# Kernel optimization log

Measured on AMD Instinct MI355X. Metric: run time of the kernel, lower is better.

Reference implementation:

```python
import jax, jax.numpy as jnp
import numpy as np

N = 50000   # nodes
E = 800000  # edges (avg degree 16)
D = 64      # isize == hidden_dim
L = 3       # num_gc_layers
BN_EPS = 1e-5


def setup_inputs() -> dict:
    key = jax.random.key(0)
    ks = jax.random.split(key, 8)
    x = jax.random.normal(ks[0], (N, D), dtype=jnp.float32)
    edge_index = jax.random.randint(ks[1], (2, E), 0, N, dtype=jnp.int64)
    # Stacked per-layer MLP params (layer 0 has isize==hidden_dim so shapes match)
    scale = 0.05
    W1 = jax.random.normal(ks[2], (L, D, D), dtype=jnp.float32) * scale
    b1 = jax.random.normal(ks[3], (L, D), dtype=jnp.float32) * scale
    W2 = jax.random.normal(ks[4], (L, D, D), dtype=jnp.float32) * scale
    b2 = jax.random.normal(ks[5], (L, D), dtype=jnp.float32) * scale
    gamma = jnp.ones((L, D), dtype=jnp.float32)
    beta = jnp.zeros((L, D), dtype=jnp.float32)
    return {"x": x, "edge_index": edge_index, "W1": W1, "b1": b1,
            "W2": W2, "b2": b2, "gamma": gamma, "beta": beta}


def reference(x, edge_index, W1, b1, W2, b2, gamma, beta):
    # GINConv (eps=0): h_i' = MLP(x_i + sum_{j->i} x_j), then BatchNorm1d
    # (training-mode batch statistics), ReLU on all but the last layer.
    # Dropout is identity (deterministic / eval).
    src = edge_index[0]
    dst = edge_index[1]
    h = x
    for i in range(L):
        agg = jax.ops.segment_sum(h[src], dst, num_segments=N)  # [N, D] scatter-add
        z = h + agg                                             # (1+eps)*x + agg, eps=0
        z = jnp.maximum(z @ W1[i] + b1[i], 0.0)                 # MLP hidden + ReLU
        z = z @ W2[i] + b2[i]                                   # MLP out
        mean = jnp.mean(z, axis=0)
        var = jnp.var(z, axis=0)                                # biased var, as torch BN
        z = (z - mean) * jax.lax.rsqrt(var + BN_EPS) * gamma[i] + beta[i]
        if i < L - 1:
            z = jnp.maximum(z, 0.0)
        h = z
    return h
```

## Files before the change

### kernel.cpp

```cpp
#include <hip/hip_runtime.h>

#define NN 50000
#define NPAD 50064
#define EE 800000
#define DD 64
#define BN_EPS 1e-5f

#define NPART 8
#define PART_NODES 6250
#define CAP 64
#define BCAP 131072
#define NSCAT 32
#define NB_BUCKET 782
#define NB_AGG  12500
#define NB_MLP  782
#define NB_SETUP 1563
#define NB_ELT8 1563
#define NB_APPLY 3125

typedef __attribute__((ext_vector_type(8))) short short8v;
typedef __attribute__((ext_vector_type(4))) float float4v;

__device__ __forceinline__ unsigned bfpack2(float a, float b) {
    union { float f; unsigned u; } ua, ub;
    ua.f = a; ub.f = b;
    unsigned ra = ua.u + 0x7fffu + ((ua.u >> 16) & 1u);
    unsigned rb = ub.u + 0x7fffu + ((ub.u >> 16) & 1u);
    return (ra >> 16) | (rb & 0xffff0000u);
}

__device__ __forceinline__ unsigned short bf16of(float v) {
    union { float f; unsigned u; } x; x.f = v;
    unsigned r = x.u + 0x7fffu + ((x.u >> 16) & 1u);
    return (unsigned short)(r >> 16);
}

__global__ __launch_bounds__(256) void k_setup(const float* __restrict__ x,
                                               unsigned* __restrict__ xb,
                                               const float* __restrict__ W1,
                                               const float* __restrict__ W2,
                                               unsigned short* __restrict__ Wb,
                                               int* __restrict__ bucketCnt,
                                               float* __restrict__ stats) {
    int t = blockIdx.x * 256 + threadIdx.x;
    if (t < NN * 8) {
        const float4* p = (const float4*)(x + (size_t)t * 8);
        float4 a = p[0], b = p[1];
        uint4 o;
        o.x = bfpack2(a.x, a.y); o.y = bfpack2(a.z, a.w);
        o.z = bfpack2(b.x, b.y); o.w = bfpack2(b.z, b.w);
        ((uint4*)xb)[t] = o;
    }
    if (t < 3 * 2 * 4096) {
        int l = t / 8192;
        int rem = t - l * 8192;
        int m = rem / 4096;
        int e = rem - m * 4096;
        int c = e >> 6, k = e & 63;
        const float* W = (m == 0 ? W1 : W2) + l * 4096;
        Wb[t] = bf16of(W[k * 64 + c]);
    }
    if (t < 128) bucketCnt[t] = 0;
    else if (t < 512) stats[t - 128] = 0.f;
}

__global__ __launch_bounds__(1024) void k_build(const int* __restrict__ src,
                                                const int* __restrict__ dst,
                                                unsigned long long* __restrict__ bucket,
                                                int* __restrict__ bucketCnt,
                                                int* __restrict__ cursor) {
    __shared__ int lcnt[8];
    __shared__ int lbase[8];
    int t = threadIdx.x;
    int g = blockIdx.x * 1024 + t;
    if (g < NN) cursor[g] = 0;
    if (t < 8) lcnt[t] = 0;
    __syncthreads();
    int d = 0, s = 0, p = 0, loc = 0;
    bool ok = (g < EE);
    if (ok) {
        d = __builtin_nontemporal_load(dst + g);
        s = __builtin_nontemporal_load(src + g);
        p = (unsigned)d / PART_NODES;
        loc = atomicAdd(&lcnt[p], 1);
    }
    __syncthreads();
    if (t < 8) lbase[t] = atomicAdd(&bucketCnt[t * 16], lcnt[t]);
    __syncthreads();
    if (ok) {
        unsigned long long v = ((unsigned long long)(unsigned)s << 32) | (unsigned)d;
        bucket[(size_t)p * BCAP + lbase[p] + loc] = v;
    }
}

__global__ __launch_bounds__(256) void k_scatter(const unsigned long long* __restrict__ bucket,
                                                 const int* __restrict__ bucketCnt,
                                                 int* __restrict__ cursor,
                                                 int* __restrict__ col) {
    int p = blockIdx.x & 7;
    int cnt = bucketCnt[p * 16];
    const unsigned long long* b = bucket + (size_t)p * BCAP;
    for (int i = (blockIdx.x >> 3) * 256 + threadIdx.x; i < cnt; i += NSCAT * 256) {
        unsigned long long v = __builtin_nontemporal_load(b + i);
        int d = (int)(v & 0xffffffffu);
        int s = (int)(v >> 32);
        int pos = atomicAdd(&cursor[d], 1);
        col[d * CAP + pos] = s;
    }
}

__global__ __launch_bounds__(256) void k_agg4(const unsigned* __restrict__ hb,
                                              const int* __restrict__ deg,
                                              const int* __restrict__ col,
                                              unsigned* __restrict__ outZb) {
    int node = blockIdx.x * 4 + (threadIdx.x >> 6);
    int lane = threadIdx.x & 63;
    int li = lane & 7;
    int slot = lane >> 3;
    int dn = deg[node];
    int base = node * CAP;
    const uint4* hb4 = (const uint4*)hb;
    float acc[8];
#pragma unroll
    for (int i = 0; i < 8; ++i) acc[i] = 0.f;

#define UNPK_ADD(U)                                                      \
    {                                                                    \
        uint4 _u = (U);                                                  \
        union { unsigned u; float f; } l0, h0, l1, h1, l2, h2, l3, h3;   \
        l0.u = _u.x << 16; h0.u = _u.x & 0xffff0000u;                    \
        l1.u = _u.y << 16; h1.u = _u.y & 0xffff0000u;                    \
        l2.u = _u.z << 16; h2.u = _u.z & 0xffff0000u;                    \
        l3.u = _u.w << 16; h3.u = _u.w & 0xffff0000u;                    \
        acc[0] += l0.f; acc[1] += h0.f; acc[2] += l1.f; acc[3] += h1.f;  \
        acc[4] += l2.f; acc[5] += h2.f; acc[6] += l3.f; acc[7] += h3.f;  \
    }

    if (slot == 0)
        UNPK_ADD(hb4[(size_t)node * 8 + li]);

    int k = slot;
    for (; k + 8 < dn; k += 16) {
        int s0 = __builtin_nontemporal_load(col + base + k);
        int s1 = __builtin_nontemporal_load(col + base + k + 8);
        uint4 u0 = hb4[(size_t)s0 * 8 + li];
        uint4 u1 = hb4[(size_t)s1 * 8 + li];
        UNPK_ADD(u0);
        UNPK_ADD(u1);
    }
    if (k < dn) {
        int s0 = __builtin_nontemporal_load(col + base + k);
        UNPK_ADD(hb4[(size_t)s0 * 8 + li]);
    }
#undef UNPK_ADD

#pragma unroll
    for (int i = 0; i < 8; ++i) acc[i] += __shfl_xor(acc[i], 8);
#pragma unroll
    for (int i = 0; i < 8; ++i) acc[i] += __shfl_xor(acc[i], 16);
#pragma unroll
    for (int i = 0; i < 8; ++i) acc[i] += __shfl_xor(acc[i], 32);

    if (slot == 0) {
        uint4 o;
        o.x = bfpack2(acc[0], acc[1]);
        o.y = bfpack2(acc[2], acc[3]);
        o.z = bfpack2(acc[4], acc[5]);
        o.w = bfpack2(acc[6], acc[7]);
        ((uint4*)outZb)[(size_t)node * 8 + li] = o;
    }
}

__global__ __launch_bounds__(256) void k_mlp_mfma(const unsigned short* __restrict__ Zb,
                                                  const unsigned short* __restrict__ WbL,
                                                  const float* __restrict__ b1,
                                                  const float* __restrict__ b2,
                                                  float* __restrict__ Zf,
                                                  float* __restrict__ statsL) {
    __shared__ unsigned short sm[4][16 * 72];
    __shared__ float sred[2][4][64];
    int w = threadIdx.x >> 6;
    int lane = threadIdx.x & 63;
    int q = lane >> 4;
    int cl = lane & 15;
    int r0 = blockIdx.x * 64 + w * 16;

    short8v B1[4][2], B2[4][2];
#pragma unroll
    for (int t = 0; t < 4; ++t) {
#pragma unroll
        for (int h = 0; h < 2; ++h) {
            B1[t][h] = *(const short8v*)(WbL + ((t * 16 + cl) * 64 + h * 32 + q * 8));
            B2[t][h] = *(const short8v*)(WbL + 4096 + ((t * 16 + cl) * 64 + h * 32 + q * 8));
        }
    }

    const unsigned short* zr = Zb + (size_t)(r0 + cl) * 64;
    short8v a0 = *(const short8v*)(zr + q * 8);
    short8v a1 = *(const short8v*)(zr + 32 + q * 8);

    float4v acc1[4];
#pragma unroll
    for (int t = 0; t < 4; ++t) {
        float b = b1[t * 16 + cl];
        acc1[t] = (float4v){b, b, b, b};
        acc1[t] = __builtin_amdgcn_mfma_f32_16x16x32_bf16(a0, B1[t][0], acc1[t], 0, 0, 0);
        acc1[t] = __builtin_amdgcn_mfma_f32_16x16x32_bf16(a1, B1[t][1], acc1[t], 0, 0, 0);
    }

    unsigned short* s = sm[w];
#pragma unroll
    for (int t = 0; t < 4; ++t) {
#pragma unroll
        for (int r = 0; r < 4; ++r) {
            float v = fmaxf(acc1[t][r], 0.f);
            s[(q * 4 + r) * 72 + t * 16 + cl] = bf16of(v);
        }
    }

    short8v a2_0 = *(const short8v*)(s + cl * 72 + q * 8);
    short8v a2_1 = *(const short8v*)(s + cl * 72 + 32 + q * 8);

    float4v acc2[4];
#pragma unroll
    for (int t = 0; t < 4; ++t) {
        float b = b2[t * 16 + cl];
        acc2[t] = (float4v){b, b, b, b};
        acc2[t] = __builtin_amdgcn_mfma_f32_16x16x32_bf16(a2_0, B2[t][0], acc2[t], 0, 0, 0);
        acc2[t] = __builtin_amdgcn_mfma_f32_16x16x32_bf16(a2_1, B2[t][1], acc2[t], 0, 0, 0);
    }

#pragma unroll
    for (int t = 0; t < 4; ++t) {
#pragma unroll
        for (int r = 0; r < 4; ++r) {
            int row = r0 + q * 4 + r;
            if (row < NN) Zf[(size_t)row * 64 + t * 16 + cl] = acc2[t][r];
        }
    }

#pragma unroll
    for (int t = 0; t < 4; ++t) {
        float sv = 0.f, qv = 0.f;
#pragma unroll
        for (int r = 0; r < 4; ++r) {
            int row = r0 + q * 4 + r;
            float v = (row < NN) ? acc2[t][r] : 0.f;
            sv += v;
            qv = fmaf(v, v, qv);
        }
        sv += __shfl_xor(sv, 16); sv += __shfl_xor(sv, 32);
        qv += __shfl_xor(qv, 16); qv += __shfl_xor(qv, 32);
        if (lane < 16) {
            sred[0][w][t * 16 + cl] = sv;
            sred[1][w][t * 16 + cl] = qv;
        }
    }
    __syncthreads();
    int tt = threadIdx.x;
    if (tt < 128) {
        int which = tt >> 6, c = tt & 63;
        float tot = sred[which][0][c] + sred[which][1][c] +
                    sred[which][2][c] + sred[which][3][c];
        atomicAdd(&statsL[which * 64 + c], tot);
    }
}

__global__ __launch_bounds__(256) void k_bnapply16(const float* __restrict__ Z,
                                                   const float* __restrict__ statsL,
                                                   const float* __restrict__ gammaL,
                                                   const float* __restrict__ betaL,
                                                   unsigned* __restrict__ hb) {
    __shared__ float sa[64];
    __shared__ float sc[64];
    int tt = threadIdx.x;
    if (tt < 64) {
        float mean = statsL[tt] * (1.f / NN);
        float var = statsL[64 + tt] * (1.f / NN) - mean * mean;
        float a = gammaL[tt] * rsqrtf(var + BN_EPS);
        sa[tt] = a;
        sc[tt] = fmaf(-mean, a, betaL[tt]);
    }
    __syncthreads();
    int t = blockIdx.x * 256 + tt;
    if (t >= NN * 8) return;
    int cb = (t & 7) * 8;
    const float4* p = (const float4*)(Z + (size_t)t * 8);
    float4 a = p[0], b = p[1];
    a.x = fmaxf(fmaf(a.x, sa[cb + 0], sc[cb + 0]), 0.f);
    a.y = fmaxf(fmaf(a.y, sa[cb + 1], sc[cb + 1]), 0.f);
    a.z = fmaxf(fmaf(a.z, sa[cb + 2], sc[cb + 2]), 0.f);
    a.w = fmaxf(fmaf(a.w, sa[cb + 3], sc[cb + 3]), 0.f);
    b.x = fmaxf(fmaf(b.x, sa[cb + 4], sc[cb + 4]), 0.f);
    b.y = fmaxf(fmaf(b.y, sa[cb + 5], sc[cb + 5]), 0.f);
    b.z = fmaxf(fmaf(b.z, sa[cb + 6], sc[cb + 6]), 0.f);
    b.w = fmaxf(fmaf(b.w, sa[cb + 7], sc[cb + 7]), 0.f);
    uint4 o;
    o.x = bfpack2(a.x, a.y); o.y = bfpack2(a.z, a.w);
    o.z = bfpack2(b.x, b.y); o.w = bfpack2(b.z, b.w);
    ((uint4*)hb)[t] = o;
}

__global__ __launch_bounds__(256) void k_apply_aff(const float* __restrict__ B,
                                                   const float* __restrict__ statsL,
                                                   const float* __restrict__ gammaL,
                                                   const float* __restrict__ betaL,
                                                   float* __restrict__ out) {
    __shared__ float sa[64];
    __shared__ float sc[64];
    int t = threadIdx.x;
    if (t < 64) {
        float mean = statsL[t] * (1.f / NN);
        float var = statsL[64 + t] * (1.f / NN) - mean * mean;
        float a = gammaL[t] * rsqrtf(var + BN_EPS);
        sa[t] = a;
        sc[t] = fmaf(-mean, a, betaL[t]);
    }
    __syncthreads();
    int i4 = blockIdx.x * 256 + t;
    if (i4 >= NN * 16) return;
    int cb = (i4 & 15) * 4;
    float4 v = ((const float4*)B)[i4];
    float4 o;
    o.x = fmaf(v.x, sa[cb + 0], sc[cb + 0]);
    o.y = fmaf(v.y, sa[cb + 1], sc[cb + 1]);
    o.z = fmaf(v.z, sa[cb + 2], sc[cb + 2]);
    o.w = fmaf(v.w, sa[cb + 3], sc[cb + 3]);
    ((float4*)out)[i4] = o;
}

extern "C" void kernel_launch(void* const* d_in, const int* in_sizes, int n_in,
                              void* d_out, int out_size, void* d_ws, size_t ws_size,
                              hipStream_t stream) {
    const float* x     = (const float*)d_in[0];
    const int*   ei    = (const int*)d_in[1];
    const float* W1    = (const float*)d_in[2];
    const float* b1    = (const float*)d_in[3];
    const float* W2    = (const float*)d_in[4];
    const float* b2    = (const float*)d_in[5];
    const float* gamma = (const float*)d_in[6];
    const float* beta  = (const float*)d_in[7];
    float* out = (float*)d_out;

    const int* src = ei;
    const int* dst = ei + EE;

    char* w = (char*)d_ws;
    unsigned*       Zb  = (unsigned*)w;       w += (size_t)NPAD * DD * 2;
    float*          Zf  = (float*)w;          w += (size_t)NN * DD * 4;
    unsigned*       Hb  = (unsigned*)w;       w += (size_t)NN * DD * 2;
    unsigned*       Xb  = (unsigned*)w;       w += (size_t)NN * DD * 2;
    int*            col = (int*)w;            w += (size_t)NN * CAP * 4;
    unsigned long long* bucket = (unsigned long long*)w;
    w += (size_t)NPART * BCAP * 8;
    int*            cursor    = (int*)w;      w += (size_t)NN * 4;
    int*            bucketCnt = (int*)w;      w += 128 * 4;
    float*          stats     = (float*)w;    w += 384 * 4;
    unsigned short* Wb        = (unsigned short*)w; w += 3 * 2 * 4096 * 2;

    k_setup<<<NB_SETUP, 256, 0, stream>>>(x, Xb, W1, W2, Wb, bucketCnt, stats);
    k_build<<<NB_BUCKET, 1024, 0, stream>>>(src, dst, bucket, bucketCnt, cursor);
    k_scatter<<<NPART * NSCAT, 256, 0, stream>>>(bucket, bucketCnt, cursor, col);

    k_agg4<<<NB_AGG, 256, 0, stream>>>(Xb, cursor, col, Zb);
    k_mlp_mfma<<<NB_MLP, 256, 0, stream>>>((unsigned short*)Zb, Wb, b1, b2, Zf, stats);
    k_bnapply16<<<NB_ELT8, 256, 0, stream>>>(Zf, stats, gamma, beta, Hb);

    k_agg4<<<NB_AGG, 256, 0, stream>>>(Hb, cursor, col, Zb);
    k_mlp_mfma<<<NB_MLP, 256, 0, stream>>>((unsigned short*)Zb, Wb + 8192, b1 + 64, b2 + 64, Zf, stats + 128);
    k_bnapply16<<<NB_ELT8, 256, 0, stream>>>(Zf, stats + 128, gamma + 64, beta + 64, Hb);

    k_agg4<<<NB_AGG, 256, 0, stream>>>(Hb, cursor, col, Zb);
    k_mlp_mfma<<<NB_MLP, 256, 0, stream>>>((unsigned short*)Zb, Wb + 16384, b1 + 128, b2 + 128, Zf, stats + 256);
    k_apply_aff<<<NB_APPLY, 256, 0, stream>>>(Zf, stats + 256, gamma + 128, beta + 128, out);
}
```

Before: 239.5 us.

## Fuse BatchNorm apply and ReLU into neighbor aggregation, store MLP output as bf16

Drops the separate BN-apply kernels for layers 0 and 1. The MLP kernel now writes its pre-BN output as bf16 through shared-memory staging. The next aggregation kernel then applies the affine BN and ReLU to every gathered neighbor row on the fly. This removes one full fp32 write plus read-and-write pass per layer and two launches. In exchange it adds per-edge FMA and max work, plus an extra bf16 rounding step before BN is applied.

```diff
diff --git a/kernel.cpp b/kernel.cpp
--- a/kernel.cpp
+++ b/kernel.cpp
@@ -15,7 +15,6 @@
 #define NB_AGG  12500
 #define NB_MLP  782
 #define NB_SETUP 1563
-#define NB_ELT8 1563
 #define NB_APPLY 3125
 
 typedef __attribute__((ext_vector_type(8))) short short8v;
@@ -109,10 +108,27 @@
     }
 }
 
+template<int FUSE>
 __global__ __launch_bounds__(256) void k_agg4(const unsigned* __restrict__ hb,
                                               const int* __restrict__ deg,
                                               const int* __restrict__ col,
+                                              const float* __restrict__ statsL,
+                                              const float* __restrict__ gammaL,
+                                              const float* __restrict__ betaL,
                                               unsigned* __restrict__ outZb) {
+    __shared__ float sa[64];
+    __shared__ float sc[64];
+    if (FUSE) {
+        int tt = threadIdx.x;
+        if (tt < 64) {
+            float mean = statsL[tt] * (1.f / NN);
+            float var = statsL[64 + tt] * (1.f / NN) - mean * mean;
+            float a = gammaL[tt] * rsqrtf(var + BN_EPS);
+            sa[tt] = a;
+            sc[tt] = fmaf(-mean, a, betaL[tt]);
+        }
+        __syncthreads();
+    }
     int node = blockIdx.x * 4 + (threadIdx.x >> 6);
     int lane = threadIdx.x & 63;
     int li = lane & 7;
@@ -120,6 +136,11 @@
     int dn = deg[node];
     int base = node * CAP;
     const uint4* hb4 = (const uint4*)hb;
+    float a8[8], c8[8];
+    if (FUSE) {
+#pragma unroll
+        for (int j = 0; j < 8; ++j) { a8[j] = sa[li * 8 + j]; c8[j] = sc[li * 8 + j]; }
+    }
     float acc[8];
 #pragma unroll
     for (int i = 0; i < 8; ++i) acc[i] = 0.f;
@@ -132,8 +153,10 @@
         l1.u = _u.y << 16; h1.u = _u.y & 0xffff0000u;                    \
         l2.u = _u.z << 16; h2.u = _u.z & 0xffff0000u;                    \
         l3.u = _u.w << 16; h3.u = _u.w & 0xffff0000u;                    \
-        acc[0] += l0.f; acc[1] += h0.f; acc[2] += l1.f; acc[3] += h1.f;  \
-        acc[4] += l2.f; acc[5] += h2.f; acc[6] += l3.f; acc[7] += h3.f;  \
+        float v[8] = {l0.f, h0.f, l1.f, h1.f, l2.f, h2.f, l3.f, h3.f};   \
+        _Pragma("unroll")                                                \
+        for (int j = 0; j < 8; ++j)                                      \
+            acc[j] += FUSE ? fmaxf(fmaf(v[j], a8[j], c8[j]), 0.f) : v[j];\
     }
 
     if (slot == 0)
@@ -171,10 +194,12 @@
     }
 }
 
+template<int OUTF32>
 __global__ __launch_bounds__(256) void k_mlp_mfma(const unsigned short* __restrict__ Zb,
                                                   const unsigned short* __restrict__ WbL,
                                                   const float* __restrict__ b1,
                                                   const float* __restrict__ b2,
+                                                  unsigned short* __restrict__ Mb,
                                                   float* __restrict__ Zf,
                                                   float* __restrict__ statsL) {
     __shared__ unsigned short sm[4][16 * 72];
@@ -230,12 +255,29 @@
         acc2[t] = __builtin_amdgcn_mfma_f32_16x16x32_bf16(a2_1, B2[t][1], acc2[t], 0, 0, 0);
     }
 
-#pragma unroll
-    for (int t = 0; t < 4; ++t) {
-#pragma unroll
-        for (int r = 0; r < 4; ++r) {
-            int row = r0 + q * 4 + r;
-            if (row < NN) Zf[(size_t)row * 64 + t * 16 + cl] = acc2[t][r];
+    if (OUTF32) {
+#pragma unroll
+        for (int t = 0; t < 4; ++t) {
+#pragma unroll
+            for (int r = 0; r < 4; ++r) {
+                int row = r0 + q * 4 + r;
+                if (row < NN) Zf[(size_t)row * 64 + t * 16 + cl] = acc2[t][r];
+            }
+        }
+    } else {
+#pragma unroll
+        for (int t = 0; t < 4; ++t) {
+#pragma unroll
+            for (int r = 0; r < 4; ++r) {
+                s[(q * 4 + r) * 72 + t * 16 + cl] = bf16of(acc2[t][r]);
+            }
+        }
+        short8v m0 = *(const short8v*)(s + cl * 72 + q * 8);
+        short8v m1 = *(const short8v*)(s + cl * 72 + 32 + q * 8);
+        int orow = r0 + cl;
+        if (orow < NN) {
+            *(short8v*)(Mb + (size_t)orow * 64 + q * 8) = m0;
+            *(short8v*)(Mb + (size_t)orow * 64 + 32 + q * 8) = m1;
         }
     }
 
@@ -264,41 +306,6 @@
                     sred[which][2][c] + sred[which][3][c];
         atomicAdd(&statsL[which * 64 + c], tot);
     }
-}
-
-__global__ __launch_bounds__(256) void k_bnapply16(const float* __restrict__ Z,
-                                                   const float* __restrict__ statsL,
-                                                   const float* __restrict__ gammaL,
-                                                   const float* __restrict__ betaL,
-                                                   unsigned* __restrict__ hb) {
-    __shared__ float sa[64];
-    __shared__ float sc[64];
-    int tt = threadIdx.x;
-    if (tt < 64) {
-        float mean = statsL[tt] * (1.f / NN);
-        float var = statsL[64 + tt] * (1.f / NN) - mean * mean;
-        float a = gammaL[tt] * rsqrtf(var + BN_EPS);
-        sa[tt] = a;
-        sc[tt] = fmaf(-mean, a, betaL[tt]);
-    }
-    __syncthreads();
-    int t = blockIdx.x * 256 + tt;
-    if (t >= NN * 8) return;
-    int cb = (t & 7) * 8;
-    const float4* p = (const float4*)(Z + (size_t)t * 8);
-    float4 a = p[0], b = p[1];
-    a.x = fmaxf(fmaf(a.x, sa[cb + 0], sc[cb + 0]), 0.f);
-    a.y = fmaxf(fmaf(a.y, sa[cb + 1], sc[cb + 1]), 0.f);
-    a.z = fmaxf(fmaf(a.z, sa[cb + 2], sc[cb + 2]), 0.f);
-    a.w = fmaxf(fmaf(a.w, sa[cb + 3], sc[cb + 3]), 0.f);
-    b.x = fmaxf(fmaf(b.x, sa[cb + 4], sc[cb + 4]), 0.f);
-    b.y = fmaxf(fmaf(b.y, sa[cb + 5], sc[cb + 5]), 0.f);
-    b.z = fmaxf(fmaf(b.z, sa[cb + 6], sc[cb + 6]), 0.f);
-    b.w = fmaxf(fmaf(b.w, sa[cb + 7], sc[cb + 7]), 0.f);
-    uint4 o;
-    o.x = bfpack2(a.x, a.y); o.y = bfpack2(a.z, a.w);
-    o.z = bfpack2(b.x, b.y); o.w = bfpack2(b.z, b.w);
-    ((uint4*)hb)[t] = o;
 }
 
 __global__ __launch_bounds__(256) void k_apply_aff(const float* __restrict__ B,
@@ -346,10 +353,10 @@
     const int* dst = ei + EE;
 
     char* w = (char*)d_ws;
-    unsigned*       Zb  = (unsigned*)w;       w += (size_t)NPAD * DD * 2;
+    unsigned*       Ab  = (unsigned*)w;       w += (size_t)NPAD * DD * 2;
+    unsigned*       Mb  = (unsigned*)w;       w += (size_t)NPAD * DD * 2;
+    unsigned*       Xb  = (unsigned*)w;       w += (size_t)NPAD * DD * 2;
     float*          Zf  = (float*)w;          w += (size_t)NN * DD * 4;
-    unsigned*       Hb  = (unsigned*)w;       w += (size_t)NN * DD * 2;
-    unsigned*       Xb  = (unsigned*)w;       w += (size_t)NN * DD * 2;
     int*            col = (int*)w;            w += (size_t)NN * CAP * 4;
     unsigned long long* bucket = (unsigned long long*)w;
     w += (size_t)NPART * BCAP * 8;
@@ -362,15 +369,16 @@
     k_build<<<NB_BUCKET, 1024, 0, stream>>>(src, dst, bucket, bucketCnt, cursor);
     k_scatter<<<NPART * NSCAT, 256, 0, stream>>>(bucket, bucketCnt, cursor, col);
 
-    k_agg4<<<NB_AGG, 256, 0, stream>>>(Xb, cursor, col, Zb);
-    k_mlp_mfma<<<NB_MLP, 256, 0, stream>>>((unsigned short*)Zb, Wb, b1, b2, Zf, stats);
-    k_bnapply16<<<NB_ELT8, 256, 0, stream>>>(Zf, stats, gamma, beta, Hb);
-
-    k_agg4<<<NB_AGG, 256, 0, stream>>>(Hb, cursor, col, Zb);
-    k_mlp_mfma<<<NB_MLP, 256, 0, stream>>>((unsigned short*)Zb, Wb + 8192, b1 + 64, b2 + 64, Zf, stats + 128);
-    k_bnapply16<<<NB_ELT8, 256, 0, stream>>>(Zf, stats + 128, gamma + 64, beta + 64, Hb);
-
-    k_agg4<<<NB_AGG, 256, 0, stream>>>(Hb, cursor, col, Zb);
-    k_mlp_mfma<<<NB_MLP, 256, 0, stream>>>((unsigned short*)Zb, Wb + 16384, b1 + 128, b2 + 128, Zf, stats + 256);
+    k_agg4<0><<<NB_AGG, 256, 0, stream>>>(Xb, cursor, col, nullptr, nullptr, nullptr, Ab);
+    k_mlp_mfma<0><<<NB_MLP, 256, 0, stream>>>((unsigned short*)Ab, Wb, b1, b2,
+                                              (unsigned short*)Mb, nullptr, stats);
+
+    k_agg4<1><<<NB_AGG, 256, 0, stream>>>(Mb, cursor, col, stats, gamma, beta, Ab);
+    k_mlp_mfma<0><<<NB_MLP, 256, 0, stream>>>((unsigned short*)Ab, Wb + 8192, b1 + 64, b2 + 64,
+                                              (unsigned short*)Mb, nullptr, stats + 128);
+
+    k_agg4<1><<<NB_AGG, 256, 0, stream>>>(Mb, cursor, col, stats + 128, gamma + 64, beta + 64, Ab);
+    k_mlp_mfma<1><<<NB_MLP, 256, 0, stream>>>((unsigned short*)Ab, Wb + 16384, b1 + 128, b2 + 128,
+                                              nullptr, Zf, stats + 256);
     k_apply_aff<<<NB_APPLY, 256, 0, stream>>>(Zf, stats + 256, gamma + 128, beta + 128, out);
 }
```

Result: no change. 234.9 us (-1.9%).
